# Optimization experiments

Measured on AMD Instinct MI355X. Metric: run time of the kernel, lower is better.

The kernel has to match this reference:

```python
import jax, jax.numpy as jnp
import numpy as np

DIM = 1024
NUM_HEADS = 16
HEAD_DIM = DIM // NUM_HEADS


def setup_inputs() -> dict:
    key = jax.random.key(0)
    k_x, k_qkv, k_proj, k_pb = jax.random.split(key, 4)
    B, N, C = 4, 2048, DIM
    x = jax.random.normal(k_x, (B, N, C), dtype=jnp.float32)
    # Dense 'qkv': kernel [C, 3C], no bias (qkv_bias=False)
    W_qkv = jax.random.normal(k_qkv, (C, 3 * C), dtype=jnp.float32) * (C ** -0.5)
    # Dense 'proj': kernel [C, C] + bias [C] (proj_bias=True)
    W_proj = jax.random.normal(k_proj, (C, C), dtype=jnp.float32) * (C ** -0.5)
    b_proj = jax.random.normal(k_pb, (C,), dtype=jnp.float32) * 0.01
    return {"x": x, "W_qkv": W_qkv, "W_proj": W_proj, "b_proj": b_proj}


def reference(x, W_qkv, W_proj, b_proj):
    B, N, C = x.shape
    H, D = NUM_HEADS, HEAD_DIM
    scale = D ** -0.5
    qkv = x @ W_qkv  # [B, N, 3C]
    qkv = qkv.reshape(B, N, 3, H, D).transpose(2, 0, 3, 1, 4)  # [3, B, H, N, D]
    q, k, v = qkv[0], qkv[1], qkv[2]
    attn = jnp.einsum('bhnd,bhmd->bhnm', q, k) * scale  # [B, H, N, N]
    attn = jax.nn.softmax(attn, axis=-1)
    out = jnp.einsum('bhnm,bhmd->bhnd', attn, v)  # [B, H, N, D]
    out = out.transpose(0, 2, 1, 3).reshape(B, N, C)
    return out @ W_proj + b_proj
```

## Files before the change

kernel.cpp:

```cpp
#include <hip/hip_runtime.h>
#include <hip/hip_bf16.h>
#include <cstdint>
#include <cstddef>

#define C_DIM 1024
#define N_HEADS 16
#define H_DIM 64
#define N_BATCH 4
#define SEQ_LEN 2048
#define N_BH 64
#define M_ROWS 8192

typedef __attribute__((ext_vector_type(8))) short bf16x8;
typedef __attribute__((ext_vector_type(4))) float f32x4;
typedef __attribute__((ext_vector_type(8))) float f32x8;
typedef __attribute__((ext_vector_type(2))) float f32x2;
typedef __attribute__((ext_vector_type(16))) float f32x16;
typedef __attribute__((ext_vector_type(4))) unsigned short us4;
typedef __attribute__((ext_vector_type(8))) unsigned short us8;
typedef __attribute__((ext_vector_type(4))) float fl4;

__device__ __forceinline__ unsigned short f2bf(float f) {
  union { float f; unsigned u; } v; v.f = f;
  unsigned r = (v.u + 0x7FFFu + ((v.u >> 16) & 1u)) >> 16;
  return (unsigned short)r;
}

__device__ __forceinline__ unsigned pk2(float a, float b) {
  union { __hip_bfloat162 h2; unsigned u; } c;
  c.h2 = __float22bfloat162_rn(float2{a, b});
  return c.u;
}

__device__ __forceinline__ void gload16(const void* g, void* l) {
  __builtin_amdgcn_global_load_lds(
      (const __attribute__((address_space(1))) unsigned int*)g,
      (__attribute__((address_space(3))) unsigned int*)l, 16, 0, 0);
}

__global__ void cast_x_kernel(const float* __restrict__ in,
                              unsigned short* __restrict__ out, int n8) {
  int i = blockIdx.x * blockDim.x + threadIdx.x;
  if (i >= n8) return;
  const fl4* p = reinterpret_cast<const fl4*>(in) + (size_t)i * 2;
  fl4 a = p[0], b = p[1];
  us8 w;
  w[0] = f2bf(a[0]); w[1] = f2bf(a[1]); w[2] = f2bf(a[2]); w[3] = f2bf(a[3]);
  w[4] = f2bf(b[0]); w[5] = f2bf(b[1]); w[6] = f2bf(b[2]); w[7] = f2bf(b[3]);
  *(reinterpret_cast<us8*>(out) + i) = w;
}

__global__ void transpose_cast_kernel(const float* __restrict__ in,
                                      unsigned short* __restrict__ out,
                                      int R, int C) {
  __shared__ float tile[64][65];
  int t = threadIdx.x;
  int tc = blockIdx.x * 64;
  int tr = blockIdx.y * 64;
  int hi = t >> 4, lo = t & 15;
#pragma unroll
  for (int i = 0; i < 4; ++i) {
    int r = i * 16 + hi;
    int c = lo * 4;
    fl4 v = *reinterpret_cast<const fl4*>(&in[(size_t)(tr + r) * C + tc + c]);
    tile[c + 0][r] = v[0]; tile[c + 1][r] = v[1];
    tile[c + 2][r] = v[2]; tile[c + 3][r] = v[3];
  }
  __syncthreads();
#pragma unroll
  for (int i = 0; i < 4; ++i) {
    int c = i * 16 + hi;
    int r = lo * 4;
    us4 w;
    w[0] = f2bf(tile[c][r + 0]); w[1] = f2bf(tile[c][r + 1]);
    w[2] = f2bf(tile[c][r + 2]); w[3] = f2bf(tile[c][r + 3]);
    *reinterpret_cast<us4*>(&out[(size_t)(tc + c) * R + tr + r]) = w;
  }
}

template <int EPI>
__global__ __launch_bounds__(256, 3) void gemm_v2_kernel(
    const unsigned short* __restrict__ A, const unsigned short* __restrict__ Bt,
    unsigned short* __restrict__ outQ, unsigned short* __restrict__ outK,
    unsigned short* __restrict__ outV, float* __restrict__ outF,
    const float* __restrict__ bias, int K) {
  __shared__ __attribute__((aligned(16))) char lds[3 * 16384];
  const int tid = threadIdx.x;
  const int lane = tid & 63, wave = tid >> 6;
  const int wr = wave >> 1, wn = wave & 1;
  const int brow = blockIdx.y * 128;
  const int bcol = blockIdx.x * 128;
  const int rr = lane & 15, g = lane >> 4;

  const int rbase =
      (rr >> 1) * 128 + (((((rr & 1) << 2) | g) ^ (rr >> 1)) << 4);

  const int s1 = tid + 256;
  const int l0 = tid >> 3, v0 = (tid & 7) ^ (l0 & 7);
  const int l1 = s1 >> 3, v1 = (s1 & 7) ^ (l1 & 7);
  const int m0 = 2 * l0 + (v0 >> 2), g0 = v0 & 3;
  const int m1 = 2 * l1 + (v1 >> 2), g1 = v1 & 3;
  const char* srcA0 = (const char*)(A + (size_t)(brow + m0) * K + g0 * 8);
  const char* srcA1 = (const char*)(A + (size_t)(brow + m1) * K + g1 * 8);
  const char* srcB0 = (const char*)(Bt + (size_t)(bcol + m0) * K + g0 * 8);
  const char* srcB1 = (const char*)(Bt + (size_t)(bcol + m1) * K + g1 * 8);
  const int oA0 = wave * 1024 + (lane & 63) * 16;
  const int oA1 = oA0 + 4096;
  const int oB0 = oA0 + 8192;
  const int oB1 = oA0 + 12288;

  f32x4 acc[4][4];
#pragma unroll
  for (int m = 0; m < 4; ++m)
#pragma unroll
    for (int n = 0; n < 4; ++n) acc[m][n] = (f32x4){0.f, 0.f, 0.f, 0.f};

  const int NT = K >> 5;

#pragma unroll
  for (int pt = 0; pt < 2; ++pt) {
    char* bb = lds + pt * 16384;
    size_t ko = (size_t)pt * 64;
    gload16(srcA0 + ko, bb + oA0);
    gload16(srcA1 + ko, bb + oA1);
    gload16(srcB0 + ko, bb + oB0);
    gload16(srcB1 + ko, bb + oB1);
  }

  int rbuf = 0, nbuf = 2;
  for (int kt = 0; kt < NT; ++kt) {
    if (kt < NT - 1) {
      asm volatile("s_waitcnt vmcnt(4)" ::: "memory");
    } else {
      asm volatile("s_waitcnt vmcnt(0)" ::: "memory");
    }
    __builtin_amdgcn_sched_barrier(0);
    __builtin_amdgcn_s_barrier();
    __builtin_amdgcn_sched_barrier(0);
    if (kt + 2 < NT) {
      char* bb = lds + nbuf * 16384;
      size_t ko = (size_t)(kt + 2) * 64;
      gload16(srcA0 + ko, bb + oA0);
      gload16(srcA1 + ko, bb + oA1);
      gload16(srcB0 + ko, bb + oB0);
      gload16(srcB1 + ko, bb + oB1);
    }
    const char* rb = lds + rbuf * 16384;
    bf16x8 af[4], bf[4];
#pragma unroll
    for (int fm = 0; fm < 4; ++fm)
      af[fm] = *reinterpret_cast<const bf16x8*>(rb + wr * 4096 + fm * 1024 +
                                                rbase);
#pragma unroll
    for (int fn = 0; fn < 4; ++fn)
      bf[fn] = *reinterpret_cast<const bf16x8*>(rb + 8192 + wn * 4096 +
                                                fn * 1024 + rbase);
    asm volatile("s_waitcnt lgkmcnt(0)" ::: "memory");
    __builtin_amdgcn_sched_barrier(0);
    __builtin_amdgcn_s_setprio(1);
#pragma unroll
    for (int fm = 0; fm < 4; ++fm)
#pragma unroll
      for (int fn = 0; fn < 4; ++fn)
        acc[fm][fn] = __builtin_amdgcn_mfma_f32_16x16x32_bf16(
            af[fm], bf[fn], acc[fm][fn], 0, 0, 0);
    __builtin_amdgcn_s_setprio(0);
    rbuf = rbuf == 2 ? 0 : rbuf + 1;
    nbuf = nbuf == 2 ? 0 : nbuf + 1;
  }

  if (EPI == 0) {
    int part = bcol >> 10;
#pragma unroll
    for (int fn = 0; fn < 4; ++fn) {
      int col = (bcol & 1023) + wn * 64 + fn * 16 + rr;
      int h = col >> 6, d = col & 63;
#pragma unroll
      for (int fm = 0; fm < 4; ++fm) {
        int rowb = brow + wr * 64 + fm * 16 + g * 4;
        int b = rowb >> 11, nr = rowb & 2047;
        size_t bhbase = (size_t)(b * N_HEADS + h) << 17;
        if (part == 0) {
#pragma unroll
          for (int r = 0; r < 4; ++r)
            outQ[bhbase + (size_t)(nr + r) * H_DIM + d] =
                f2bf(acc[fm][fn][r] * 0.1803368801111837f);
        } else if (part == 1) {
          int ks = d >> 4, lhi = (d >> 3) & 1, j = d & 7;
#pragma unroll
          for (int r = 0; r < 4; ++r) {
            int n = nr + r;
            int t = n >> 5, ln = (n & 31) + (lhi << 5);
            outK[bhbase + (size_t)(((t * 4 + ks) * 64 + ln) * 8 + j)] =
                f2bf(acc[fm][fn][r]);
          }
        } else {
          int dt = d >> 5, m = (nr >> 4) & 1, t = nr >> 5;
          int ln = (d & 31) + (((nr >> 3) & 1) << 5);
          int j0 = nr & 7;
          us4 w;
#pragma unroll
          for (int r = 0; r < 4; ++r) w[r] = f2bf(acc[fm][fn][r]);
          *reinterpret_cast<us4*>(
              &outV[bhbase +
                    (size_t)(((t * 4 + dt * 2 + m) * 64 + ln) * 8 + j0)]) = w;
        }
      }
    }
  } else {
#pragma unroll
    for (int fn = 0; fn < 4; ++fn) {
      int col = bcol + wn * 64 + fn * 16 + rr;
      float bv = bias[col];
#pragma unroll
      for (int fm = 0; fm < 4; ++fm) {
        int rowb = brow + wr * 64 + fm * 16 + g * 4;
#pragma unroll
        for (int r = 0; r < 4; ++r)
          outF[(size_t)(rowb + r) * C_DIM + col] = acc[fm][fn][r] + bv;
      }
    }
  }
}

__global__ __launch_bounds__(256) void attn_kernel(
    const unsigned short* __restrict__ Qs, const unsigned short* __restrict__ Kf,
    const unsigned short* __restrict__ Vf, unsigned short* __restrict__ Oo) {
  const int tid = threadIdx.x;
  const int lane = tid & 63, wave = tid >> 6;
  const int l31 = lane & 31, h5 = lane >> 5;
  int i = blockIdx.x;
  int bh = (i & 7) * 8 + ((i >> 3) & 7);
  int qb = i >> 6;
  const int q0 = qb * 128 + wave * 32;
  const int bb = bh >> 4, hh = bh & 15;

  const unsigned short* Qb = Qs + ((size_t)bh << 17);
  const char* Kb = (const char*)Kf + ((size_t)bh << 18) + lane * 16;
  const char* Vb = (const char*)Vf + ((size_t)bh << 18) + lane * 16;

  bf16x8 qf[4];
#pragma unroll
  for (int ks = 0; ks < 4; ++ks)
    qf[ks] = *reinterpret_cast<const bf16x8*>(
        &Qb[(size_t)(q0 + l31) * H_DIM + ks * 16 + h5 * 8]);

  f32x16 oacc[2];
#pragma unroll
  for (int dt = 0; dt < 2; ++dt)
#pragma unroll
    for (int r = 0; r < 16; ++r) oacc[dt][r] = 0.f;
  float lsum = 0.f;

  f32x16 z16;
#pragma unroll
  for (int r = 0; r < 16; ++r) z16[r] = 0.f;

#pragma unroll 2
  for (int t = 0; t < 64; ++t) {
    const char* kp = Kb + t * 4096;
    const char* vp = Vb + t * 4096;
    bf16x8 kfr[4], vfr[2][2];
#pragma unroll
    for (int ks = 0; ks < 4; ++ks)
      kfr[ks] = *reinterpret_cast<const bf16x8*>(kp + ks * 1024);
#pragma unroll
    for (int dt = 0; dt < 2; ++dt)
#pragma unroll
      for (int m = 0; m < 2; ++m)
        vfr[dt][m] =
            *reinterpret_cast<const bf16x8*>(vp + dt * 2048 + m * 1024);

    __builtin_amdgcn_s_setprio(1);
    f32x16 sa =
        __builtin_amdgcn_mfma_f32_32x32x16_bf16(kfr[0], qf[0], z16, 0, 0, 0);
#pragma unroll
    for (int ks = 1; ks < 4; ++ks)
      sa = __builtin_amdgcn_mfma_f32_32x32x16_bf16(kfr[ks], qf[ks], sa, 0, 0, 0);
    __builtin_amdgcn_s_setprio(0);
    f32x16 pv;
#pragma unroll
    for (int r = 0; r < 16; ++r) pv[r] = __builtin_amdgcn_exp2f(sa[r]);
    {
      f32x8 h8 = __builtin_shufflevector(pv, pv, 0, 1, 2, 3, 4, 5, 6, 7) +
                 __builtin_shufflevector(pv, pv, 8, 9, 10, 11, 12, 13, 14, 15);
      f32x4 h4 = __builtin_shufflevector(h8, h8, 0, 1, 2, 3) +
                 __builtin_shufflevector(h8, h8, 4, 5, 6, 7);
      f32x2 h2 = __builtin_shufflevector(h4, h4, 0, 1) +
                 __builtin_shufflevector(h4, h4, 2, 3);
      lsum += h2[0] + h2[1];
    }
    unsigned X0 = pk2(pv[0], pv[1]), X1 = pk2(pv[2], pv[3]);
    unsigned X2 = pk2(pv[4], pv[5]), X3 = pk2(pv[6], pv[7]);
    unsigned X4 = pk2(pv[8], pv[9]), X5 = pk2(pv[10], pv[11]);
    unsigned X6 = pk2(pv[12], pv[13]), X7 = pk2(pv[14], pv[15]);
    asm("v_permlane32_swap_b32 %0, %1" : "+v"(X0), "+v"(X2));
    asm("v_permlane32_swap_b32 %0, %1" : "+v"(X1), "+v"(X3));
    asm("v_permlane32_swap_b32 %0, %1" : "+v"(X4), "+v"(X6));
    asm("v_permlane32_swap_b32 %0, %1" : "+v"(X5), "+v"(X7));
    union { unsigned u[4]; bf16x8 v; } pf0, pf1;
    pf0.u[0] = X0; pf0.u[1] = X1; pf0.u[2] = X2; pf0.u[3] = X3;
    pf1.u[0] = X4; pf1.u[1] = X5; pf1.u[2] = X6; pf1.u[3] = X7;
    __builtin_amdgcn_s_setprio(1);
#pragma unroll
    for (int dt = 0; dt < 2; ++dt) {
      oacc[dt] = __builtin_amdgcn_mfma_f32_32x32x16_bf16(vfr[dt][0], pf0.v,
                                                         oacc[dt], 0, 0, 0);
      oacc[dt] = __builtin_amdgcn_mfma_f32_32x32x16_bf16(vfr[dt][1], pf1.v,
                                                         oacc[dt], 0, 0, 0);
    }
    __builtin_amdgcn_s_setprio(0);
  }

  lsum += __shfl_xor(lsum, 32);
  float inv = 1.f / lsum;
  int n = q0 + l31;
  unsigned short* orow = Oo + ((size_t)bb * SEQ_LEN + n) * C_DIM + hh * H_DIM;
#pragma unroll
  for (int dt = 0; dt < 2; ++dt)
#pragma unroll
    for (int G = 0; G < 4; ++G) {
      us4 w;
#pragma unroll
      for (int u = 0; u < 4; ++u) w[u] = f2bf(oacc[dt][G * 4 + u] * inv);
      *reinterpret_cast<us4*>(&orow[dt * 32 + G * 8 + h5 * 4]) = w;
    }
}

extern "C" void kernel_launch(void* const* d_in, const int* in_sizes, int n_in,
                              void* d_out, int out_size, void* d_ws,
                              size_t ws_size, hipStream_t stream) {
  const float* x = (const float*)d_in[0];
  const float* Wqkv = (const float*)d_in[1];
  const float* Wproj = (const float*)d_in[2];
  const float* bproj = (const float*)d_in[3];
  float* out = (float*)d_out;

  unsigned short* xbf = (unsigned short*)d_ws;
  unsigned short* Wtqkv = xbf + (size_t)M_ROWS * C_DIM;
  unsigned short* Wtproj = Wtqkv + (size_t)3 * C_DIM * C_DIM;
  unsigned short* Qb = Wtproj + (size_t)C_DIM * C_DIM;
  unsigned short* Kbf = Qb + (size_t)N_BH * SEQ_LEN * H_DIM;
  unsigned short* Vbf = Kbf + (size_t)N_BH * SEQ_LEN * H_DIM;
  unsigned short* Ob = xbf;

  cast_x_kernel<<<4096, 256, 0, stream>>>(x, xbf, M_ROWS * C_DIM / 8);
  transpose_cast_kernel<<<dim3(48, 16), 256, 0, stream>>>(Wqkv, Wtqkv, C_DIM,
                                                          3 * C_DIM);
  transpose_cast_kernel<<<dim3(16, 16), 256, 0, stream>>>(Wproj, Wtproj, C_DIM,
                                                          C_DIM);
  gemm_v2_kernel<0><<<dim3(24, 64), 256, 0, stream>>>(
      xbf, Wtqkv, Qb, Kbf, Vbf, nullptr, nullptr, C_DIM);
  attn_kernel<<<dim3(1024), 256, 0, stream>>>(Qb, Kbf, Vbf, Ob);
  gemm_v2_kernel<1><<<dim3(8, 64), 256, 0, stream>>>(
      Ob, Wtproj, nullptr, nullptr, nullptr, out, bproj, C_DIM);
}
```

Before: 203.0 us.

## Split attention KV loop across two wave groups and merge partials via LDS

Each attention block now has 8 waves instead of 4. The second group of four waves handles the second half of the key/value sequence for the same query rows, and both groups finish by combining their partial output accumulators and row sums through shared memory. This doubles the parallelism per query tile to hide K/V load latency and raise occupancy. The cost is an LDS reduction, a block-wide barrier and higher per-block resource use. The bf16 packing helper is also replaced with inline v_cvt_pk_bf16_f32 instructions.

```diff
diff --git a/kernel.cpp b/kernel.cpp
--- a/kernel.cpp
+++ b/kernel.cpp
@@ -24,12 +24,6 @@
   union { float f; unsigned u; } v; v.f = f;
   unsigned r = (v.u + 0x7FFFu + ((v.u >> 16) & 1u)) >> 16;
   return (unsigned short)r;
-}
-
-__device__ __forceinline__ unsigned pk2(float a, float b) {
-  union { __hip_bfloat162 h2; unsigned u; } c;
-  c.h2 = __float22bfloat162_rn(float2{a, b});
-  return c.u;
 }
 
 __device__ __forceinline__ void gload16(const void* g, void* l) {
@@ -223,21 +217,25 @@
   }
 }
 
-__global__ __launch_bounds__(256) void attn_kernel(
+__global__ __launch_bounds__(512) void attn_kernel(
     const unsigned short* __restrict__ Qs, const unsigned short* __restrict__ Kf,
     const unsigned short* __restrict__ Vf, unsigned short* __restrict__ Oo) {
+  __shared__ float plds[4][64][33];
   const int tid = threadIdx.x;
   const int lane = tid & 63, wave = tid >> 6;
+  const int qw = wave & 3, half = wave >> 2;
   const int l31 = lane & 31, h5 = lane >> 5;
   int i = blockIdx.x;
   int bh = (i & 7) * 8 + ((i >> 3) & 7);
   int qb = i >> 6;
-  const int q0 = qb * 128 + wave * 32;
+  const int q0 = qb * 128 + qw * 32;
   const int bb = bh >> 4, hh = bh & 15;
 
   const unsigned short* Qb = Qs + ((size_t)bh << 17);
-  const char* Kb = (const char*)Kf + ((size_t)bh << 18) + lane * 16;
-  const char* Vb = (const char*)Vf + ((size_t)bh << 18) + lane * 16;
+  const char* Kb =
+      (const char*)Kf + ((size_t)bh << 18) + lane * 16 + half * 131072;
+  const char* Vb =
+      (const char*)Vf + ((size_t)bh << 18) + lane * 16 + half * 131072;
 
   bf16x8 qf[4];
 #pragma unroll
@@ -257,7 +255,7 @@
   for (int r = 0; r < 16; ++r) z16[r] = 0.f;
 
 #pragma unroll 2
-  for (int t = 0; t < 64; ++t) {
+  for (int t = 0; t < 32; ++t) {
     const char* kp = Kb + t * 4096;
     const char* vp = Vb + t * 4096;
     bf16x8 kfr[4], vfr[2][2];
@@ -290,10 +288,15 @@
                  __builtin_shufflevector(h4, h4, 2, 3);
       lsum += h2[0] + h2[1];
     }
-    unsigned X0 = pk2(pv[0], pv[1]), X1 = pk2(pv[2], pv[3]);
-    unsigned X2 = pk2(pv[4], pv[5]), X3 = pk2(pv[6], pv[7]);
-    unsigned X4 = pk2(pv[8], pv[9]), X5 = pk2(pv[10], pv[11]);
-    unsigned X6 = pk2(pv[12], pv[13]), X7 = pk2(pv[14], pv[15]);
+    unsigned X0, X1, X2, X3, X4, X5, X6, X7;
+    asm("v_cvt_pk_bf16_f32 %0, %1, %2" : "=v"(X0) : "v"(pv[0]), "v"(pv[1]));
+    asm("v_cvt_pk_bf16_f32 %0, %1, %2" : "=v"(X1) : "v"(pv[2]), "v"(pv[3]));
+    asm("v_cvt_pk_bf16_f32 %0, %1, %2" : "=v"(X2) : "v"(pv[4]), "v"(pv[5]));
+    asm("v_cvt_pk_bf16_f32 %0, %1, %2" : "=v"(X3) : "v"(pv[6]), "v"(pv[7]));
+    asm("v_cvt_pk_bf16_f32 %0, %1, %2" : "=v"(X4) : "v"(pv[8]), "v"(pv[9]));
+    asm("v_cvt_pk_bf16_f32 %0, %1, %2" : "=v"(X5) : "v"(pv[10]), "v"(pv[11]));
+    asm("v_cvt_pk_bf16_f32 %0, %1, %2" : "=v"(X6) : "v"(pv[12]), "v"(pv[13]));
+    asm("v_cvt_pk_bf16_f32 %0, %1, %2" : "=v"(X7) : "v"(pv[14]), "v"(pv[15]));
     asm("v_permlane32_swap_b32 %0, %1" : "+v"(X0), "+v"(X2));
     asm("v_permlane32_swap_b32 %0, %1" : "+v"(X1), "+v"(X3));
     asm("v_permlane32_swap_b32 %0, %1" : "+v"(X4), "+v"(X6));
@@ -312,6 +315,25 @@
     __builtin_amdgcn_s_setprio(0);
   }
 
+  if (half) {
+    float* p = &plds[qw][lane][0];
+#pragma unroll
+    for (int dt = 0; dt < 2; ++dt)
+#pragma unroll
+      for (int r = 0; r < 16; ++r) p[dt * 16 + r] = oacc[dt][r];
+    p[32] = lsum;
+  }
+  __syncthreads();
+  if (half) return;
+  {
+    const float* p = &plds[qw][lane][0];
+#pragma unroll
+    for (int dt = 0; dt < 2; ++dt)
+#pragma unroll
+      for (int r = 0; r < 16; ++r) oacc[dt][r] += p[dt * 16 + r];
+    lsum += p[32];
+  }
+
   lsum += __shfl_xor(lsum, 32);
   float inv = 1.f / lsum;
   int n = q0 + l31;
@@ -351,7 +373,7 @@
                                                           C_DIM);
   gemm_v2_kernel<0><<<dim3(24, 64), 256, 0, stream>>>(
       xbf, Wtqkv, Qb, Kbf, Vbf, nullptr, nullptr, C_DIM);
-  attn_kernel<<<dim3(1024), 256, 0, stream>>>(Qb, Kbf, Vbf, Ob);
+  attn_kernel<<<dim3(1024), 512, 0, stream>>>(Qb, Kbf, Vbf, Ob);
   gemm_v2_kernel<1><<<dim3(8, 64), 256, 0, stream>>>(
       Ob, Wtproj, nullptr, nullptr, nullptr, out, bproj, C_DIM);
 }
```

Measured after the change: 195.1 us. 1.04x faster.
